# Performance work log

Hardware: AMD Instinct MI355X
Metric: run time of the kernel (lower is better)

## Reference

```python
import jax, jax.numpy as jnp
import numpy as np

B, S, IN, N, OUT = 4, 4096, 1024, 1024, 1024  # state_size == num_heads, head_dim = 1, hippo D = 1


def setup_inputs() -> dict:
    key = jax.random.key(0)
    ks = jax.random.split(key, 6)
    x = jax.random.normal(ks[0], (B, S, IN), dtype=jnp.float32)
    # input_projection: Linear(input_size, state_size, bias=True)
    Wi = jax.random.normal(ks[1], (IN, N), dtype=jnp.float32) / np.sqrt(IN)
    bi = jax.random.normal(ks[2], (N,), dtype=jnp.float32) * 0.01
    # state_weight (N,1,1) -> per-head scalar recurrence weight; hippo_weight (N,1) -> per-head scalar
    w = jax.random.normal(ks[3], (N,), dtype=jnp.float32)
    u = jax.random.normal(ks[4], (N,), dtype=jnp.float32)
    # output_projection: Linear(state_size, output_size, bias=False)
    Wo = jax.random.normal(ks[5], (N, OUT), dtype=jnp.float32) / np.sqrt(N)
    input_state = jnp.zeros((B, N), dtype=jnp.float32)         # (B, N, H=1) squeezed
    hippo_state = jnp.zeros((B, N, 1, 1), dtype=jnp.float32)   # (B, N, H=1, D=1)
    return {"x": x, "Wi": Wi, "bi": bi, "w": w, "u": u, "Wo": Wo,
            "input_state": input_state, "hippo_state": hippo_state}


def reference(x, Wi, bi, w, u, Wo, input_state, hippo_state):
    # input projection then split into N heads of dim 1 -> [B, S, N]
    xp = jnp.einsum("bsi,in->bsn", x, Wi) + bi
    # hippo cross-term: (hippo_state @ hippo_weight) with H=D=1 -> scalar per (b, n).
    # hippo_state is never updated inside the recurrence (torch path), so this is constant over time.
    hippo_term = hippo_state[..., 0, 0] * u  # [B, N]

    def step(h, xt):
        # h_t = tanh(h_{t-1} * w + x_t + hippo_term)   (per-head scalar recurrence, H=1)
        h = jnp.tanh(h * w + xt + hippo_term)
        return h, h

    xs = jnp.swapaxes(xp, 0, 1)  # [S, B, N]
    last_state, ys = jax.lax.scan(step, input_state, xs)
    states = jnp.swapaxes(ys, 0, 1)  # [B, S, N]
    out = jnp.einsum("bsn,no->bso", states, Wo)  # output_projection (no bias)
    output_state = last_state.reshape(B, -1)     # input[:, -1] flattened over (N, H)
    return out, output_state
```

## Files before the change

### kernel.cpp

```cpp
#include <hip/hip_runtime.h>
#include <hip/hip_bf16.h>

using f16x8 = __attribute__((ext_vector_type(8))) _Float16;
using f32x4 = __attribute__((ext_vector_type(4))) float;

extern "C" __device__ float __ocml_native_exp2_f32(float);

static constexpr int Bc = 4, Sc = 4096, INc = 1024, Nc = 1024, OUTc = 1024;
static constexpr int Mc = Bc * Sc;
#define K2LE 2.8853900817779268f

__device__ __forceinline__ unsigned short f2h(float f) {
    return __builtin_bit_cast(unsigned short, (_Float16)f);
}
__device__ __forceinline__ float h2f(unsigned short s) {
    return (float)__builtin_bit_cast(_Float16, s);
}

__global__ __launch_bounds__(256) void tr_h2(const float* __restrict__ Wi,
                                             const float* __restrict__ Wo,
                                             unsigned short* __restrict__ WiT,
                                             unsigned short* __restrict__ WoT) {
    __shared__ float t[32][33];
    const float* in = blockIdx.z ? Wo : Wi;
    unsigned short* out = blockIdx.z ? WoT : WiT;
    int c0 = blockIdx.x * 32, r0 = blockIdx.y * 32;
    for (int i = threadIdx.y; i < 32; i += 8)
        t[i][threadIdx.x] = in[(size_t)(r0 + i) * 1024 + c0 + threadIdx.x];
    __syncthreads();
    for (int i = threadIdx.y; i < 32; i += 8)
        out[(size_t)(c0 + i) * 1024 + r0 + threadIdx.x] = f2h(t[threadIdx.x][i]);
}

template<int MODE>
__global__ __launch_bounds__(256) void gemm_h(const unsigned short* __restrict__ Ah16,
                                              const float* __restrict__ Af32,
                                              const unsigned short* __restrict__ BT,
                                              float* __restrict__ C, int N, int K,
                                              const float* __restrict__ bi,
                                              const float* __restrict__ u,
                                              const float* __restrict__ hs,
                                              const float* __restrict__ wv) {
    constexpr int BM = 128, BN = 128, BK = 64;
    __shared__ alignas(16) unsigned short Ash[BM * BK];
    __shared__ alignas(16) unsigned short Asl[MODE ? BM * BK : 1];
    __shared__ alignas(16) unsigned short Bs[BN * BK];
    const int nb = N >> 7;
    const int cpx = (int)gridDim.x >> 3;
    const int wg = (blockIdx.x & 7) * cpx + (blockIdx.x >> 3);
    const int bm = wg / nb, bn = wg % nb;
    const int tid = threadIdx.x;
    const int w = tid >> 6, l = tid & 63;
    const int wr = w >> 1, wc = w & 1;
    const int r = l & 15, g4 = l >> 4;
    const int lrow = l >> 3, lcol = (l & 7) * 8;

    f32x4 acc[4][4] = {};

    const size_t boff = (size_t)bn * BN * K;

    for (int k0 = 0; k0 < K; k0 += BK) {
        __syncthreads();
#pragma unroll
        for (int i = 0; i < 4; i++) {
            size_t grow = (size_t)((w * 4 + i) * 8 + lrow) * K + (k0 + lcol);
            int ldst = (w * 4 + i) * 512;
            __builtin_amdgcn_global_load_lds(
                (const __attribute__((address_space(1))) void*)(BT + boff + grow),
                (__attribute__((address_space(3))) void*)(Bs + ldst), 16, 0, 0);
        }
        if (MODE) {
            float4 av[8];
#pragma unroll
            for (int i = 0; i < 8; i++) {
                int rg = (w * 8 + i) * 4 + (l >> 4);
                av[i] = *reinterpret_cast<const float4*>(
                    Af32 + (size_t)(bm * BM + rg) * K + k0 + (l & 15) * 4);
            }
#pragma unroll
            for (int i = 0; i < 8; i++) {
                int rg = (w * 8 + i) * 4 + (l >> 4);
                int off = rg * BK + (l & 15) * 4;
                float fx0 = av[i].x, fx1 = av[i].y, fx2 = av[i].z, fx3 = av[i].w;
                unsigned short h0s = f2h(fx0), h1s = f2h(fx1), h2s = f2h(fx2), h3s = f2h(fx3);
                ushort4 hh = { h0s, h1s, h2s, h3s };
                ushort4 ll = { f2h(fx0 - h2f(h0s)), f2h(fx1 - h2f(h1s)),
                               f2h(fx2 - h2f(h2s)), f2h(fx3 - h2f(h3s)) };
                *reinterpret_cast<ushort4*>(Ash + off) = hh;
                *reinterpret_cast<ushort4*>(Asl + off) = ll;
            }
        } else {
            const size_t aoff = (size_t)bm * BM * K;
#pragma unroll
            for (int i = 0; i < 4; i++) {
                size_t grow = (size_t)((w * 4 + i) * 8 + lrow) * K + (k0 + lcol);
                __builtin_amdgcn_global_load_lds(
                    (const __attribute__((address_space(1))) void*)(Ah16 + aoff + grow),
                    (__attribute__((address_space(3))) void*)(Ash + (w * 4 + i) * 512), 16, 0, 0);
            }
        }
        __syncthreads();
#pragma unroll
        for (int kk = 0; kk < BK; kk += 32) {
            f16x8 ah[4], al[4], bf[4];
#pragma unroll
            for (int m = 0; m < 4; m++) {
                int off = (wr * 64 + m * 16 + r) * BK + kk + g4 * 8;
                ah[m] = *reinterpret_cast<const f16x8*>(Ash + off);
                if (MODE) al[m] = *reinterpret_cast<const f16x8*>(Asl + off);
            }
#pragma unroll
            for (int n = 0; n < 4; n++)
                bf[n] = *reinterpret_cast<const f16x8*>(Bs + (wc * 64 + n * 16 + r) * BK + kk + g4 * 8);
#pragma unroll
            for (int m = 0; m < 4; m++)
#pragma unroll
                for (int n = 0; n < 4; n++) {
                    acc[m][n] = __builtin_amdgcn_mfma_f32_16x16x32_f16(ah[m], bf[n], acc[m][n], 0, 0, 0);
                    if (MODE)
                        acc[m][n] = __builtin_amdgcn_mfma_f32_16x16x32_f16(al[m], bf[n], acc[m][n], 0, 0, 0);
                }
        }
    }

    const int bbase = MODE ? ((bm * BM) / Sc) * Nc : 0;
#pragma unroll
    for (int m = 0; m < 4; m++) {
        int row = bm * BM + wr * 64 + m * 16 + g4 * 4;
#pragma unroll
        for (int n = 0; n < 4; n++) {
            int col = bn * BN + wc * 64 + n * 16 + r;
            float extra = 0.f;
            if (MODE) extra = bi[col] + hs[bbase + col] * u[col] + wv[col];
#pragma unroll
            for (int q = 0; q < 4; q++) {
                float v = acc[m][n][q];
                if (MODE) v = (v + extra) * K2LE;
                C[(size_t)(row + q) * N + col] = v;
            }
        }
    }
}

static constexpr int SROW = 68;

template<bool PREF>
__device__ __forceinline__ void sblk(const float* __restrict__ xrow,
                                     float (&cur)[32], float (&nxt)[32],
                                     float* __restrict__ hbl, int tblk, float nw2, float& rr) {
#pragma unroll
    for (int d = 0; d < 32; d++) {
        if (PREF) nxt[d] = xrow[(size_t)(tblk + 32 + d) << 10];
        float z = fmaf(nw2, rr, cur[d]);
        float e = __ocml_native_exp2_f32(z);
        rr = __builtin_amdgcn_rcpf(e + 1.f);
        hbl[d * SROW] = rr;
    }
    asm volatile("s_waitcnt lgkmcnt(0)" ::: "memory");
    __builtin_amdgcn_s_barrier();
}

__device__ __forceinline__ unsigned int pk2(float a, float b) {
    return ((unsigned int)f2h(fmaf(-2.f, b, 1.f)) << 16) | f2h(fmaf(-2.f, a, 1.f));
}

__device__ __forceinline__ void drain(const float* __restrict__ buf, int tblk,
                                      unsigned short* __restrict__ srow, int n0, int l) {
    __builtin_amdgcn_s_barrier();
    asm volatile("" ::: "memory");
    int row8 = l >> 3, cg = l & 7;
#pragma unroll
    for (int i = 0; i < 4; i++) {
        int row = i * 8 + row8;
        float4 a = *reinterpret_cast<const float4*>(&buf[row * SROW + cg * 8]);
        float4 b = *reinterpret_cast<const float4*>(&buf[row * SROW + cg * 8 + 4]);
        uint4 v = { pk2(a.x, a.y), pk2(a.z, a.w), pk2(b.x, b.y), pk2(b.z, b.w) };
        *reinterpret_cast<uint4*>(&srow[((size_t)(tblk + row) << 10) + n0 + cg * 8]) = v;
    }
}

__global__ __launch_bounds__(128) void scan4(const float* __restrict__ xp,
                                             const float* __restrict__ w,
                                             const float* __restrict__ h0,
                                             unsigned short* __restrict__ states,
                                             float* __restrict__ out_state) {
    __shared__ alignas(16) float hb[2][32 * SROW];
    const int l = threadIdx.x & 63;
    const int wave = threadIdx.x >> 6;
    const int b = blockIdx.x >> 4;
    const int n0 = (blockIdx.x & 15) * 64;

    if (wave == 0) {
        const int tid = blockIdx.x * 64 + l;
        const int n = tid & (Nc - 1);
        float nw2 = w[n] * (-2.f * K2LE);
        float rr = 0.5f - 0.5f * h0[tid];
        const float* xrow = xp + ((size_t)b << 22) + n;
        float* hbl0 = &hb[0][l];
        float* hbl1 = &hb[1][l];

        float xa[32], xb[32];
#pragma unroll
        for (int d = 0; d < 32; d++) xa[d] = xrow[(size_t)d << 10];

        int t = 0;
        for (; t + 64 < Sc; t += 64) {
            sblk<true>(xrow, xa, xb, hbl0, t, nw2, rr);
            sblk<true>(xrow, xb, xa, hbl1, t + 32, nw2, rr);
        }
        sblk<true >(xrow, xa, xb, hbl0, t, nw2, rr);
        sblk<false>(xrow, xb, xa, hbl1, t + 32, nw2, rr);
        out_state[tid] = fmaf(-2.f, rr, 1.f);
    } else {
        unsigned short* srow = states + ((size_t)b << 22);
        for (int t = 0; t < Sc; t += 64) {
            drain(hb[0], t, srow, n0, l);
            drain(hb[1], t + 32, srow, n0, l);
        }
    }
}

extern "C" void kernel_launch(void* const* d_in, const int* in_sizes, int n_in,
                              void* d_out, int out_size, void* d_ws, size_t ws_size,
                              hipStream_t stream) {
    const float* x  = (const float*)d_in[0];
    const float* Wi = (const float*)d_in[1];
    const float* bi = (const float*)d_in[2];
    const float* w  = (const float*)d_in[3];
    const float* u  = (const float*)d_in[4];
    const float* Wo = (const float*)d_in[5];
    const float* h0 = (const float*)d_in[6];
    const float* hs = (const float*)d_in[7];
    float* out = (float*)d_out;
    float* out_state = out + (size_t)Mc * OUTc;
    float* xp = out;

    char* ws = (char*)d_ws;
    unsigned short* states = (unsigned short*)ws;
    unsigned short* WiT = (unsigned short*)(ws + 33554432);
    unsigned short* WoT = (unsigned short*)(ws + 35651584);

    tr_h2<<<dim3(32, 32, 2), dim3(32, 8), 0, stream>>>(Wi, Wo, WiT, WoT);

    gemm_h<1><<<(Mc / 128) * (Nc / 128), 256, 0, stream>>>(nullptr, x, WiT, xp, Nc, INc, bi, u, hs, w);
    scan4<<<64, 128, 0, stream>>>(xp, w, h0, states, out_state);
    gemm_h<0><<<(Mc / 128) * (OUTc / 128), 256, 0, stream>>>(states, nullptr, WoT, out, OUTc, Nc,
                                                             nullptr, nullptr, nullptr, nullptr);
}
```

Measured before the change: 246.4 us.

## Prefetch next fp32 A tile into registers and use packed fp16 conversion

In the split-fp16 GEMM mode, the fp32 A tile loads for the next K step are now issued right after the LDS barrier, so their latency overlaps the MFMA work on the current tile. The hi/lo fp16 split also switches to packed round-toward-zero conversion (cvt_pkrtz) instead of per-element conversions. This keeps 8 float4 registers live across the compute loop, which raises register pressure. It also changes rounding from nearest to toward-zero, which slightly alters the hi/lo split.

```diff
diff --git a/kernel.cpp b/kernel.cpp
--- a/kernel.cpp
+++ b/kernel.cpp
@@ -3,6 +3,7 @@
 
 using f16x8 = __attribute__((ext_vector_type(8))) _Float16;
 using f32x4 = __attribute__((ext_vector_type(4))) float;
+using fp16x2 = __attribute__((ext_vector_type(2))) __fp16;
 
 extern "C" __device__ float __ocml_native_exp2_f32(float);
 
@@ -59,6 +60,16 @@
 
     const size_t boff = (size_t)bn * BN * K;
 
+    float4 av[8];
+    if (MODE) {
+#pragma unroll
+        for (int i = 0; i < 8; i++) {
+            int rg = (w * 8 + i) * 4 + (l >> 4);
+            av[i] = *reinterpret_cast<const float4*>(
+                Af32 + (size_t)(bm * BM + rg) * K + (l & 15) * 4);
+        }
+    }
+
     for (int k0 = 0; k0 < K; k0 += BK) {
         __syncthreads();
 #pragma unroll
@@ -70,24 +81,25 @@
                 (__attribute__((address_space(3))) void*)(Bs + ldst), 16, 0, 0);
         }
         if (MODE) {
-            float4 av[8];
-#pragma unroll
-            for (int i = 0; i < 8; i++) {
-                int rg = (w * 8 + i) * 4 + (l >> 4);
-                av[i] = *reinterpret_cast<const float4*>(
-                    Af32 + (size_t)(bm * BM + rg) * K + k0 + (l & 15) * 4);
-            }
 #pragma unroll
             for (int i = 0; i < 8; i++) {
                 int rg = (w * 8 + i) * 4 + (l >> 4);
                 int off = rg * BK + (l & 15) * 4;
                 float fx0 = av[i].x, fx1 = av[i].y, fx2 = av[i].z, fx3 = av[i].w;
-                unsigned short h0s = f2h(fx0), h1s = f2h(fx1), h2s = f2h(fx2), h3s = f2h(fx3);
-                ushort4 hh = { h0s, h1s, h2s, h3s };
-                ushort4 ll = { f2h(fx0 - h2f(h0s)), f2h(fx1 - h2f(h1s)),
-                               f2h(fx2 - h2f(h2s)), f2h(fx3 - h2f(h3s)) };
-                *reinterpret_cast<ushort4*>(Ash + off) = hh;
-                *reinterpret_cast<ushort4*>(Asl + off) = ll;
+                fp16x2 h01 = __builtin_amdgcn_cvt_pkrtz(fx0, fx1);
+                fp16x2 h23 = __builtin_amdgcn_cvt_pkrtz(fx2, fx3);
+                float r0 = fx0 - (float)h01[0];
+                float r1 = fx1 - (float)h01[1];
+                float r2 = fx2 - (float)h23[0];
+                float r3 = fx3 - (float)h23[1];
+                fp16x2 l01 = __builtin_amdgcn_cvt_pkrtz(r0, r1);
+                fp16x2 l23 = __builtin_amdgcn_cvt_pkrtz(r2, r3);
+                uint2 hh = { __builtin_bit_cast(unsigned int, h01),
+                             __builtin_bit_cast(unsigned int, h23) };
+                uint2 llv = { __builtin_bit_cast(unsigned int, l01),
+                              __builtin_bit_cast(unsigned int, l23) };
+                *reinterpret_cast<uint2*>(Ash + off) = hh;
+                *reinterpret_cast<uint2*>(Asl + off) = llv;
             }
         } else {
             const size_t aoff = (size_t)bm * BM * K;
@@ -100,6 +112,14 @@
             }
         }
         __syncthreads();
+        if (MODE && k0 + BK < K) {
+#pragma unroll
+            for (int i = 0; i < 8; i++) {
+                int rg = (w * 8 + i) * 4 + (l >> 4);
+                av[i] = *reinterpret_cast<const float4*>(
+                    Af32 + (size_t)(bm * BM + rg) * K + (k0 + BK) + (l & 15) * 4);
+            }
+        }
 #pragma unroll
         for (int kk = 0; kk < BK; kk += 32) {
             f16x8 ah[4], al[4], bf[4];
```

After: 246.1 us, median of 2. About the same (-0.1%).

## Stream fp32 A tile directly to LDS and split to fp16 hi/lo at fragment load

Applied to the files above, without the earlier changes.

In the split-precision GEMM mode, the A tile is now copied from global memory into shared memory as raw fp32 with asynchronous global_load_lds, instead of going through registers and being converted before the store. The hi/lo fp16 split is done after reading each fragment from shared memory, using packed round-toward-zero conversions. This removes the register staging and the conversion from the load path so the A load can overlap with the B load. The cost is double the shared-memory footprint and read traffic for A, plus conversion work repeated by both wave columns. The hi part now rounds toward zero rather than to nearest, but the lo residual compensates.

```diff
diff --git a/kernel.cpp b/kernel.cpp
--- a/kernel.cpp
+++ b/kernel.cpp
@@ -3,6 +3,7 @@
 
 using f16x8 = __attribute__((ext_vector_type(8))) _Float16;
 using f32x4 = __attribute__((ext_vector_type(4))) float;
+using fp16x2 = __attribute__((ext_vector_type(2))) __fp16;
 
 extern "C" __device__ float __ocml_native_exp2_f32(float);
 
@@ -42,8 +43,8 @@
                                               const float* __restrict__ hs,
                                               const float* __restrict__ wv) {
     constexpr int BM = 128, BN = 128, BK = 64;
-    __shared__ alignas(16) unsigned short Ash[BM * BK];
-    __shared__ alignas(16) unsigned short Asl[MODE ? BM * BK : 1];
+    __shared__ alignas(16) float Asf[MODE ? BM * BK : 1];
+    __shared__ alignas(16) unsigned short Ash[MODE ? 1 : BM * BK];
     __shared__ alignas(16) unsigned short Bs[BN * BK];
     const int nb = N >> 7;
     const int cpx = (int)gridDim.x >> 3;
@@ -58,6 +59,7 @@
     f32x4 acc[4][4] = {};
 
     const size_t boff = (size_t)bn * BN * K;
+    const float* Ab = MODE ? Af32 + (size_t)bm * BM * K : nullptr;
 
     for (int k0 = 0; k0 < K; k0 += BK) {
         __syncthreads();
@@ -70,24 +72,13 @@
                 (__attribute__((address_space(3))) void*)(Bs + ldst), 16, 0, 0);
         }
         if (MODE) {
-            float4 av[8];
 #pragma unroll
             for (int i = 0; i < 8; i++) {
-                int rg = (w * 8 + i) * 4 + (l >> 4);
-                av[i] = *reinterpret_cast<const float4*>(
-                    Af32 + (size_t)(bm * BM + rg) * K + k0 + (l & 15) * 4);
-            }
-#pragma unroll
-            for (int i = 0; i < 8; i++) {
-                int rg = (w * 8 + i) * 4 + (l >> 4);
-                int off = rg * BK + (l & 15) * 4;
-                float fx0 = av[i].x, fx1 = av[i].y, fx2 = av[i].z, fx3 = av[i].w;
-                unsigned short h0s = f2h(fx0), h1s = f2h(fx1), h2s = f2h(fx2), h3s = f2h(fx3);
-                ushort4 hh = { h0s, h1s, h2s, h3s };
-                ushort4 ll = { f2h(fx0 - h2f(h0s)), f2h(fx1 - h2f(h1s)),
-                               f2h(fx2 - h2f(h2s)), f2h(fx3 - h2f(h3s)) };
-                *reinterpret_cast<ushort4*>(Ash + off) = hh;
-                *reinterpret_cast<ushort4*>(Asl + off) = ll;
+                int row0 = w * 32 + i * 4;
+                size_t g = (size_t)(row0 + (l >> 4)) * K + k0 + (l & 15) * 4;
+                __builtin_amdgcn_global_load_lds(
+                    (const __attribute__((address_space(1))) void*)(Ab + g),
+                    (__attribute__((address_space(3))) void*)(Asf + row0 * BK), 16, 0, 0);
             }
         } else {
             const size_t aoff = (size_t)bm * BM * K;
@@ -105,9 +96,32 @@
             f16x8 ah[4], al[4], bf[4];
 #pragma unroll
             for (int m = 0; m < 4; m++) {
-                int off = (wr * 64 + m * 16 + r) * BK + kk + g4 * 8;
-                ah[m] = *reinterpret_cast<const f16x8*>(Ash + off);
-                if (MODE) al[m] = *reinterpret_cast<const f16x8*>(Asl + off);
+                if (MODE) {
+                    const float* ap = Asf + (wr * 64 + m * 16 + r) * BK + kk + g4 * 8;
+                    float4 a0 = *reinterpret_cast<const float4*>(ap);
+                    float4 a1 = *reinterpret_cast<const float4*>(ap + 4);
+                    fp16x2 h01 = __builtin_amdgcn_cvt_pkrtz(a0.x, a0.y);
+                    fp16x2 h23 = __builtin_amdgcn_cvt_pkrtz(a0.z, a0.w);
+                    fp16x2 h45 = __builtin_amdgcn_cvt_pkrtz(a1.x, a1.y);
+                    fp16x2 h67 = __builtin_amdgcn_cvt_pkrtz(a1.z, a1.w);
+                    fp16x2 l01 = __builtin_amdgcn_cvt_pkrtz(a0.x - (float)h01[0], a0.y - (float)h01[1]);
+                    fp16x2 l23 = __builtin_amdgcn_cvt_pkrtz(a0.z - (float)h23[0], a0.w - (float)h23[1]);
+                    fp16x2 l45 = __builtin_amdgcn_cvt_pkrtz(a1.x - (float)h45[0], a1.y - (float)h45[1]);
+                    fp16x2 l67 = __builtin_amdgcn_cvt_pkrtz(a1.z - (float)h67[0], a1.w - (float)h67[1]);
+                    uint4 hu = { __builtin_bit_cast(unsigned int, h01),
+                                 __builtin_bit_cast(unsigned int, h23),
+                                 __builtin_bit_cast(unsigned int, h45),
+                                 __builtin_bit_cast(unsigned int, h67) };
+                    uint4 lu = { __builtin_bit_cast(unsigned int, l01),
+                                 __builtin_bit_cast(unsigned int, l23),
+                                 __builtin_bit_cast(unsigned int, l45),
+                                 __builtin_bit_cast(unsigned int, l67) };
+                    ah[m] = __builtin_bit_cast(f16x8, hu);
+                    al[m] = __builtin_bit_cast(f16x8, lu);
+                } else {
+                    int off = (wr * 64 + m * 16 + r) * BK + kk + g4 * 8;
+                    ah[m] = *reinterpret_cast<const f16x8*>(Ash + off);
+                }
             }
 #pragma unroll
             for (int n = 0; n < 4; n++)
```

Result: slower. 257.1 us (+4.3%).
